# Performance work log

Hardware: AMD Instinct MI355X
Metric: run time of the kernel (lower is better)

Reference implementation:

```python
import jax, jax.numpy as jnp
import numpy as np

B, N, IN, OUT, H = 8, 1024, 256, 256, 4
D = OUT // H  # head_dim = 64


def setup_inputs() -> dict:
    key = jax.random.key(0)
    k1, k2, k3, k4 = jax.random.split(key, 4)
    h = jax.random.normal(k1, (B, N, IN), dtype=jnp.float32)
    # torch Linear weight: [out, in], Wh = h @ W.T
    W = jax.random.normal(k2, (H * D, IN), dtype=jnp.float32) * (1.0 / np.sqrt(IN))
    # attention vector a: [n_heads, 2*head_dim] (xavier-uniform-ish scale)
    a = jax.random.normal(k3, (H, 2 * D), dtype=jnp.float32) * 0.1
    adj_mask = jax.random.bernoulli(k4, 0.1, (B, N, N))
    # ensure every row has at least one neighbor (self-loop) to avoid all -inf rows
    adj_mask = adj_mask | jnp.eye(N, dtype=bool)[None]
    return {"h": h, "W": W, "a": a, "adj_mask": adj_mask}


def reference(h, W, a, adj_mask):
    # Wh: [B, H, N, D]
    Wh = (h @ W.T).reshape(B, N, H, D).transpose(0, 2, 1, 3)
    # Split 'a' into src/dst halves: e_ij = leaky_relu(a_src.Wh_i + a_dst.Wh_j)
    # (mathematically identical to the original concat+einsum, without the N^2*2D tensor)
    src = jnp.einsum('bhnd,hd->bhn', Wh, a[:, :D])
    dst = jnp.einsum('bhnd,hd->bhn', Wh, a[:, D:])
    e = jax.nn.leaky_relu(src[:, :, :, None] + dst[:, :, None, :], negative_slope=0.2)
    e = jnp.where(adj_mask[:, None, :, :], e, -jnp.inf)
    att = jax.nn.softmax(e, axis=-1)
    att = jnp.where(jnp.isnan(att), 0.0, att)
    # dropout in eval mode -> identity
    h_prime = jnp.einsum('bhij,bhjd->bhid', att, Wh)
    # concat=True: [B, N, H*D]
    return h_prime.transpose(0, 2, 1, 3).reshape(B, N, H * D)
```

## Files before the change

### kernel.cpp

```cpp
#include <hip/hip_runtime.h>
#include <hip/hip_bf16.h>

#define B 8
#define N 1024
#define IN 256
#define H 4
#define D 64
#define O 256
#define BN (B*N)

typedef __attribute__((ext_vector_type(4))) float f32x4;
typedef __attribute__((ext_vector_type(8))) short short8;
typedef __attribute__((ext_vector_type(4))) short short4v;

__device__ __forceinline__ short f2bf(float f){
  __hip_bfloat16 b = __float2bfloat16(f);
  return __builtin_bit_cast(short, b);
}
__device__ __forceinline__ float bf2f(short s){
  unsigned u = ((unsigned)(unsigned short)s) << 16;
  return __builtin_bit_cast(float, u);
}

#define PACK_BLOCKS 1024
#define CVT_BLOCKS  1056
#define H_ELEMS (BN*IN)
__global__ __launch_bounds__(256) void k_prep(const int* __restrict__ adj,
                                              unsigned* __restrict__ bits,
                                              const float* __restrict__ hmat,
                                              const float* __restrict__ Wmat,
                                              short* __restrict__ hbf,
                                              short* __restrict__ wbf){
  if(blockIdx.x < PACK_BLOCKS){
    int t = blockIdx.x * 256 + threadIdx.x;
    const int4* p = (const int4*)(adj + ((size_t)t << 5));
    unsigned word = 0;
    #pragma unroll
    for(int k = 0; k < 8; k++){
      int4 m = p[k];
      word |= (m.x != 0 ? 1u : 0u) << (k*4 + 0);
      word |= (m.y != 0 ? 1u : 0u) << (k*4 + 1);
      word |= (m.z != 0 ? 1u : 0u) << (k*4 + 2);
      word |= (m.w != 0 ? 1u : 0u) << (k*4 + 3);
    }
    bits[t] = word;
  } else {
    int idx = (blockIdx.x - PACK_BLOCKS) * 256 + threadIdx.x;
    int e = idx * 8;
    const float* srcp; short* dstp;
    if(e < H_ELEMS){ srcp = hmat + e; dstp = hbf + e; }
    else           { srcp = Wmat + (e - H_ELEMS); dstp = wbf + (e - H_ELEMS); }
    float4 a0 = *(const float4*)srcp;
    float4 a1 = *(const float4*)(srcp + 4);
    short8 pk;
    pk[0]=f2bf(a0.x); pk[1]=f2bf(a0.y); pk[2]=f2bf(a0.z); pk[3]=f2bf(a0.w);
    pk[4]=f2bf(a1.x); pk[5]=f2bf(a1.y); pk[6]=f2bf(a1.z); pk[7]=f2bf(a1.w);
    *(short8*)dstp = pk;
  }
}

__global__ __launch_bounds__(256) void k_wh(const short* __restrict__ hbf,
                                            const short* __restrict__ wbf,
                                            const float* __restrict__ avec,
                                            short* __restrict__ VT,
                                            float* __restrict__ src,
                                            float* __restrict__ dst){
  const int t = threadIdx.x;
  const int hh = t >> 6, lane = t & 63, quad = lane >> 4, l16 = lane & 15;
  const int mbase = blockIdx.x * 16;
  f32x4 acc[4];
  #pragma unroll
  for(int x=0;x<4;x++) acc[x] = (f32x4){0.f,0.f,0.f,0.f};
  const short* ap = hbf + (size_t)(mbase + l16) * IN + quad * 8;
  const short* bp0 = wbf + (size_t)(hh * 64 + l16) * IN + quad * 8;
  #pragma unroll
  for(int kk = 0; kk < 8; kk++){
    const int k0 = kk * 32;
    short8 A = *(const short8*)(ap + k0);
    #pragma unroll
    for(int dt=0; dt<4; dt++){
      short8 Bf = *(const short8*)(bp0 + (size_t)dt*16*IN + k0);
      acc[dt] = __builtin_amdgcn_mfma_f32_16x16x32_bf16(A, Bf, acc[dt], 0, 0, 0);
    }
  }
  const int bb = mbase >> 10;
  const int nb = (mbase & (N-1)) + quad * 4;
  const int bh = bb * H + hh;
  #pragma unroll
  for(int dt=0; dt<4; dt++){
    int d = dt*16 + l16;
    short4v pk;
    pk[0]=f2bf(acc[dt][0]); pk[1]=f2bf(acc[dt][1]);
    pk[2]=f2bf(acc[dt][2]); pk[3]=f2bf(acc[dt][3]);
    *(short4v*)(VT + (((size_t)bh * D + d) << 10) + nb) = pk;
  }
  float as[4], ad[4];
  #pragma unroll
  for(int dt=0; dt<4; dt++){
    as[dt] = avec[hh*(2*D) + dt*16 + l16];
    ad[dt] = avec[hh*(2*D) + D + dt*16 + l16];
  }
  #pragma unroll
  for(int r=0; r<4; r++){
    float s = 0.f, dd = 0.f;
    #pragma unroll
    for(int dt=0; dt<4; dt++){ s += acc[dt][r]*as[dt]; dd += acc[dt][r]*ad[dt]; }
    #pragma unroll
    for(int off=1; off<16; off<<=1){
      s  += __shfl_xor(s, off, 64);
      dd += __shfl_xor(dd, off, 64);
    }
    if(l16 == 0){
      int n = nb + r;
      src[(size_t)bh * N + n] = s;
      dst[(size_t)bh * N + n] = dd;
    }
  }
}

__global__ __launch_bounds__(256) void k_attn(const short* __restrict__ VT,
                                              const float* __restrict__ src,
                                              const float* __restrict__ dst,
                                              const unsigned* __restrict__ bits,
                                              float* __restrict__ pacc,
                                              float* __restrict__ plsum){
  __shared__ float dsh[512];
  const int t = threadIdx.x;
  const int wave = t >> 6, lane = t & 63, quad = lane >> 4, l16 = lane & 15;
  const int b = blockIdx.z, hh = blockIdx.y;
  const int bh = b * H + hh;
  const int ib = blockIdx.x >> 1, jc = blockIdx.x & 1;
  const int i0 = ib * 64, jbase = jc * 512;
  #pragma unroll
  for(int j = t; j < 512; j += 256) dsh[j] = dst[(size_t)bh * N + jbase + j];
  const int i = i0 + wave * 16 + l16;
  const float si = src[(size_t)bh * N + i];
  const int4* mp = (const int4*)(bits + ((size_t)b * N + i) * 32 + jc * 16);
  int4 mv0 = mp[0], mv1 = mp[1], mv2 = mp[2], mv3 = mp[3];
  unsigned mw[16] = {(unsigned)mv0.x,(unsigned)mv0.y,(unsigned)mv0.z,(unsigned)mv0.w,
                     (unsigned)mv1.x,(unsigned)mv1.y,(unsigned)mv1.z,(unsigned)mv1.w,
                     (unsigned)mv2.x,(unsigned)mv2.y,(unsigned)mv2.z,(unsigned)mv2.w,
                     (unsigned)mv3.x,(unsigned)mv3.y,(unsigned)mv3.z,(unsigned)mv3.w};
  const short* vrow = VT + (((size_t)bh * D) << 10) + jbase + quad * 8;
  f32x4 acc[4];
  #pragma unroll
  for(int x=0;x<4;x++) acc[x] = (f32x4){0.f,0.f,0.f,0.f};
  float lsum = 0.f;
  __syncthreads();
  #pragma unroll
  for(int jt = 0; jt < 16; jt++){
    const int j0 = jt * 32;
    const unsigned word = mw[jt];
    float4 d0 = *(const float4*)&dsh[j0 + quad*8];
    float4 d1 = *(const float4*)&dsh[j0 + quad*8 + 4];
    float dv[8] = {d0.x,d0.y,d0.z,d0.w,d1.x,d1.y,d1.z,d1.w};
    short8 P;
    #pragma unroll
    for(int jj=0; jj<8; jj++){
      float e = si + dv[jj];
      e = fmaxf(e, 0.2f * e);
      float p = ((word >> (quad*8 + jj)) & 1u) ? __expf(e) : 0.f;
      P[jj] = f2bf(p);
      lsum += bf2f(P[jj]);
    }
    #pragma unroll
    for(int dt=0; dt<4; dt++){
      short8 Bf = *(const short8*)(vrow + (((size_t)(dt*16 + l16)) << 10) + j0);
      acc[dt] = __builtin_amdgcn_mfma_f32_16x16x32_bf16(P, Bf, acc[dt], 0, 0, 0);
    }
  }
  lsum += __shfl_xor(lsum, 16, 64);
  lsum += __shfl_xor(lsum, 32, 64);
  const int pslot = bh * 2 + jc;
  if(quad == 0) plsum[(size_t)pslot * N + i] = lsum;
  float* pa = pacc + ((size_t)pslot << 16);
  #pragma unroll
  for(int dt=0; dt<4; dt++){
    #pragma unroll
    for(int r=0; r<4; r++){
      int ig = i0 + wave*16 + quad*4 + r;
      pa[(ig << 6) + dt*16 + l16] = acc[dt][r];
    }
  }
}

__global__ __launch_bounds__(256) void k_combine(const float* __restrict__ pacc,
                                                 const float* __restrict__ plsum,
                                                 float* __restrict__ out){
  int t = blockIdx.x * 256 + threadIdx.x;
  int o = t & 255, n = (t >> 8) & (N-1), b = t >> 18;
  int hh = o >> 6, d = o & 63;
  int slot = (b * H + hh) * 2;
  size_t base = ((size_t)slot << 16) + (n << 6) + d;
  float p = pacc[base] + pacc[base + 65536];
  float l = plsum[(size_t)slot * N + n] + plsum[(size_t)(slot+1) * N + n];
  out[t] = p / l;
}

extern "C" void kernel_launch(void* const* d_in, const int* in_sizes, int n_in,
                              void* d_out, int out_size, void* d_ws, size_t ws_size,
                              hipStream_t stream) {
  const float* hmat = (const float*)d_in[0];
  const float* Wmat = (const float*)d_in[1];
  const float* avec = (const float*)d_in[2];
  const int* adj    = (const int*)d_in[3];
  float* out = (float*)d_out;
  char* ws = (char*)d_ws;
  short*    VT    = (short*)   (ws);
  short*    hbf   = (short*)   (ws + (size_t) 4*1024*1024);
  short*    wbf   = (short*)   (ws + (size_t) 8*1024*1024);
  unsigned* bits  = (unsigned*)(ws + (size_t) 9*1024*1024);
  float*    src   = (float*)   (ws + (size_t)10*1024*1024);
  float*    dst   = (float*)   (ws + (size_t)10*1024*1024 + 131072);
  float*    plsum = (float*)   (ws + (size_t)11*1024*1024);
  float*    pacc  = (float*)   (ws + (size_t)12*1024*1024);
  k_prep<<<PACK_BLOCKS + CVT_BLOCKS, 256, 0, stream>>>(adj, bits, hmat, Wmat, hbf, wbf);
  k_wh<<<BN/16, 256, 0, stream>>>(hbf, wbf, avec, VT, src, dst);
  k_attn<<<dim3(32, H, B), 256, 0, stream>>>(VT, src, dst, bits, pacc, plsum);
  k_combine<<<(BN*O)/256, 256, 0, stream>>>(pacc, plsum, out);
}
```

Measured before the change: 138.1 us.

## Fuse combine into attention kernel by processing all columns per block

Drops the two-way split of the neighbour dimension, so each attention block covers all 1024 columns and normalizes and writes the final output directly. This removes the k_combine launch and the round trip of partial accumulators and row sums through global memory. In exchange, the attention grid halves to 512 blocks, each with a serial loop twice as long and more mask registers, which lowers parallelism.

```diff
diff --git a/kernel.cpp b/kernel.cpp
--- a/kernel.cpp
+++ b/kernel.cpp
@@ -122,33 +122,30 @@
                                               const float* __restrict__ src,
                                               const float* __restrict__ dst,
                                               const unsigned* __restrict__ bits,
-                                              float* __restrict__ pacc,
-                                              float* __restrict__ plsum){
-  __shared__ float dsh[512];
+                                              float* __restrict__ out){
+  __shared__ float dsh[N];
   const int t = threadIdx.x;
   const int wave = t >> 6, lane = t & 63, quad = lane >> 4, l16 = lane & 15;
   const int b = blockIdx.z, hh = blockIdx.y;
   const int bh = b * H + hh;
-  const int ib = blockIdx.x >> 1, jc = blockIdx.x & 1;
-  const int i0 = ib * 64, jbase = jc * 512;
-  #pragma unroll
-  for(int j = t; j < 512; j += 256) dsh[j] = dst[(size_t)bh * N + jbase + j];
+  const int i0 = blockIdx.x * 64;
+  #pragma unroll
+  for(int j = t; j < N; j += 256) dsh[j] = dst[(size_t)bh * N + j];
   const int i = i0 + wave * 16 + l16;
   const float si = src[(size_t)bh * N + i];
-  const int4* mp = (const int4*)(bits + ((size_t)b * N + i) * 32 + jc * 16);
-  int4 mv0 = mp[0], mv1 = mp[1], mv2 = mp[2], mv3 = mp[3];
-  unsigned mw[16] = {(unsigned)mv0.x,(unsigned)mv0.y,(unsigned)mv0.z,(unsigned)mv0.w,
-                     (unsigned)mv1.x,(unsigned)mv1.y,(unsigned)mv1.z,(unsigned)mv1.w,
-                     (unsigned)mv2.x,(unsigned)mv2.y,(unsigned)mv2.z,(unsigned)mv2.w,
-                     (unsigned)mv3.x,(unsigned)mv3.y,(unsigned)mv3.z,(unsigned)mv3.w};
-  const short* vrow = VT + (((size_t)bh * D) << 10) + jbase + quad * 8;
+  const int4* mp = (const int4*)(bits + ((size_t)b * N + i) * 32);
+  int4 mv[8];
+  #pragma unroll
+  for(int k=0;k<8;k++) mv[k] = mp[k];
+  const unsigned* mw = (const unsigned*)mv;
+  const short* vrow = VT + (((size_t)bh * D) << 10) + quad * 8;
   f32x4 acc[4];
   #pragma unroll
   for(int x=0;x<4;x++) acc[x] = (f32x4){0.f,0.f,0.f,0.f};
   float lsum = 0.f;
   __syncthreads();
   #pragma unroll
-  for(int jt = 0; jt < 16; jt++){
+  for(int jt = 0; jt < 32; jt++){
     const int j0 = jt * 32;
     const unsigned word = mw[jt];
     float4 d0 = *(const float4*)&dsh[j0 + quad*8];
@@ -171,30 +168,15 @@
   }
   lsum += __shfl_xor(lsum, 16, 64);
   lsum += __shfl_xor(lsum, 32, 64);
-  const int pslot = bh * 2 + jc;
-  if(quad == 0) plsum[(size_t)pslot * N + i] = lsum;
-  float* pa = pacc + ((size_t)pslot << 16);
-  #pragma unroll
-  for(int dt=0; dt<4; dt++){
-    #pragma unroll
-    for(int r=0; r<4; r++){
-      int ig = i0 + wave*16 + quad*4 + r;
-      pa[(ig << 6) + dt*16 + l16] = acc[dt][r];
-    }
-  }
-}
-
-__global__ __launch_bounds__(256) void k_combine(const float* __restrict__ pacc,
-                                                 const float* __restrict__ plsum,
-                                                 float* __restrict__ out){
-  int t = blockIdx.x * 256 + threadIdx.x;
-  int o = t & 255, n = (t >> 8) & (N-1), b = t >> 18;
-  int hh = o >> 6, d = o & 63;
-  int slot = (b * H + hh) * 2;
-  size_t base = ((size_t)slot << 16) + (n << 6) + d;
-  float p = pacc[base] + pacc[base + 65536];
-  float l = plsum[(size_t)slot * N + n] + plsum[(size_t)(slot+1) * N + n];
-  out[t] = p / l;
+  #pragma unroll
+  for(int r=0; r<4; r++){
+    float lv = __shfl(lsum, (lane & 48) + quad*4 + r, 64);
+    float inv = 1.0f / lv;
+    int ig = i0 + wave*16 + quad*4 + r;
+    float* op = out + ((size_t)b * N + ig) * O + hh * D + l16;
+    #pragma unroll
+    for(int dt=0; dt<4; dt++) op[dt*16] = acc[dt][r] * inv;
+  }
 }
 
 extern "C" void kernel_launch(void* const* d_in, const int* in_sizes, int n_in,
@@ -212,10 +194,7 @@
   unsigned* bits  = (unsigned*)(ws + (size_t) 9*1024*1024);
   float*    src   = (float*)   (ws + (size_t)10*1024*1024);
   float*    dst   = (float*)   (ws + (size_t)10*1024*1024 + 131072);
-  float*    plsum = (float*)   (ws + (size_t)11*1024*1024);
-  float*    pacc  = (float*)   (ws + (size_t)12*1024*1024);
   k_prep<<<PACK_BLOCKS + CVT_BLOCKS, 256, 0, stream>>>(adj, bits, hmat, Wmat, hbf, wbf);
   k_wh<<<BN/16, 256, 0, stream>>>(hbf, wbf, avec, VT, src, dst);
-  k_attn<<<dim3(32, H, B), 256, 0, stream>>>(VT, src, dst, bits, pacc, plsum);
-  k_combine<<<(BN*O)/256, 256, 0, stream>>>(pacc, plsum, out);
-}
+  k_attn<<<dim3(16, H, B), 256, 0, stream>>>(VT, src, dst, bits, out);
+}
```

New measurement: 139.8 us. No clear change (+1.2%).
